# Performance work log

Hardware: AMD Instinct MI355X
Metric: run time of the kernel (lower is better)

## Reference

```python
import jax, jax.numpy as jnp
import numpy as np

B, D, G, L = 8, 128, 2048, 24
GF = G // 2 + 1  # rfft bins
EPS = 1e-5


def setup_inputs() -> dict:
    key = jax.random.key(0)
    ks = jax.random.split(key, 6)
    x = jax.random.normal(ks[0], (B, D, G), dtype=jnp.float32)
    Phi_f = jax.random.normal(ks[1], (L, GF), dtype=jnp.float32) * 0.1
    Theta = jax.random.normal(ks[2], (L, D, D), dtype=jnp.float32) * (1.0 / np.sqrt(D))
    ln_gamma = jnp.ones((D,), dtype=jnp.float32)
    ln_beta = jnp.zeros((D,), dtype=jnp.float32)
    fc1_w = jax.random.normal(ks[3], (2 * D, D), dtype=jnp.float32) * (1.0 / np.sqrt(D))
    fc1_b = jnp.zeros((2 * D,), dtype=jnp.float32)
    fc2_w = jax.random.normal(ks[4], (D, 2 * D), dtype=jnp.float32) * (1.0 / np.sqrt(2 * D))
    fc2_b = jnp.zeros((D,), dtype=jnp.float32)
    return {
        'x': x, 'Phi_f': Phi_f, 'Theta': Theta,
        'ln_gamma': ln_gamma, 'ln_beta': ln_beta,
        'fc1_w': fc1_w, 'fc1_b': fc1_b, 'fc2_w': fc2_w, 'fc2_b': fc2_b,
    }


def reference(x, Phi_f, Theta, ln_gamma, ln_beta, fc1_w, fc1_b, fc2_w, fc2_b):
    # x: (B, D, G). LayerNorm over the lifting (channel) dim D.
    mean = jnp.mean(x, axis=1, keepdims=True)
    var = jnp.var(x, axis=1, keepdims=True)
    z = (x - mean) * jax.lax.rsqrt(var + EPS)
    z = z * ln_gamma[None, :, None] + ln_beta[None, :, None]

    # Spectral convolution with each Hilbert filter.
    Xf = jnp.fft.rfft(z, axis=-1)                       # (B, D, GF) complex
    Uf = Xf[:, :, None, :] * jnp.conj(Phi_f)[None, None]  # (B, D, L, GF)
    U = jnp.fft.irfft(Uf, n=G, axis=-1)                 # (B, D, L, G)

    # Per-filter channel mixing then reduction over filters:
    # einsum('bdln,lhd->bhln') followed by sum over l, fused:
    S = jnp.einsum('bdlg,lhd->bhg', U, Theta)           # (B, D, G)

    # Pointwise MLP (Conv1d kernel_size=1 == channel matmul).
    H = jnp.einsum('hd,bdg->bhg', fc1_w, S) + fc1_b[None, :, None]
    H = jax.nn.gelu(H, approximate=False)
    out = jnp.einsum('dh,bhg->bdg', fc2_w, H) + fc2_b[None, :, None]
    return x + out
```

## Files before the change

kernel.cpp:

```cpp
#include <hip/hip_runtime.h>
#include <math.h>


#define B_   8
#define D_   128
#define G_   2048
#define L_   24
#define GF_  1025
#define BD_  1024
#define DD_  16384
#define GH_  1024
#define CF_  1026
#define MF_  1088
#define MFW_ 1152
#define NF_  2048

#define PA_CV0 256
#define PA_TT0 322
#define PA_WF0 578
#define PA_WI0 1730
#define PA_END 2754

#define G1_NB  288
#define G1_END 4512

typedef __attribute__((ext_vector_type(8))) short  short8v;
typedef __attribute__((ext_vector_type(4))) float  float4v;

union FU { float f; unsigned int u; };
union V8 { short8v v; ushort u[8]; };
union V4 { uint2 p; ushort u[4]; };

static __device__ __forceinline__ float bf2f(ushort h) {
    FU v; v.u = ((unsigned int)h) << 16; return v.f;
}
static __device__ __forceinline__ ushort f2bf(float f) {
    FU v; v.f = f;
    unsigned int r = v.u + 0x7fffu + ((v.u >> 16) & 1u);
    return (ushort)(r >> 16);
}
static __device__ __forceinline__ void async16(const void* g, void* l) {
    __builtin_amdgcn_global_load_lds(
        (const __attribute__((address_space(1))) void*)g,
        (__attribute__((address_space(3))) void*)l, 16, 0, 0);
}
static __device__ __forceinline__ int is_f32(const unsigned int* graw) {
    return graw[0] == 0x3F800000u;
}

__global__ __launch_bounds__(256) void k_pre(
        const void* __restrict__ x_raw,  const void* __restrict__ th_raw,
        const unsigned int* __restrict__ graw, const void* __restrict__ be_raw,
        const void* __restrict__ w1_raw, const void* __restrict__ b1_raw,
        const void* __restrict__ w2_raw, const void* __restrict__ b2_raw,
        ushort* __restrict__ z,  ushort* __restrict__ wf,
        ushort* __restrict__ wi, ushort* __restrict__ thT,
        ushort* __restrict__ w1c, ushort* __restrict__ b1c,
        ushort* __restrict__ w2c, ushort* __restrict__ b2c) {
    __shared__ ushort T[L_][72];
    __shared__ float red[2][256];
    __shared__ float mi[2][64];
    int bid = blockIdx.x, tid = threadIdx.x;

    if (bid < PA_CV0) {
        int fl = is_f32(graw);
        int b  = bid >> 5;
        int g0 = (bid & 31) * 64;
        int gi = tid & 63, dq = tid >> 6;
        int g  = g0 + gi;
        int d0 = dq * 32;
        float vals[32];
        float s = 0.f, ss = 0.f;
        if (fl) {
            const float* xp = (const float*)x_raw + (size_t)(b * D_ + d0) * G_ + g;
            #pragma unroll 8
            for (int d = 0; d < 32; ++d) {
                float v = xp[(size_t)d * G_];
                vals[d] = v; s += v; ss += v * v;
            }
        } else {
            const ushort* xp = (const ushort*)x_raw + (size_t)(b * D_ + d0) * G_ + g;
            #pragma unroll 8
            for (int d = 0; d < 32; ++d) {
                float v = bf2f(xp[(size_t)d * G_]);
                vals[d] = v; s += v; ss += v * v;
            }
        }
        red[0][tid] = s; red[1][tid] = ss;
        __syncthreads();
        if (tid < 64) {
            float S  = red[0][tid] + red[0][tid + 64] + red[0][tid + 128] +
                       red[0][tid + 192];
            float SS = red[1][tid] + red[1][tid + 64] + red[1][tid + 128] +
                       red[1][tid + 192];
            float mean = S * (1.f / D_);
            float var  = SS * (1.f / D_) - mean * mean;
            mi[0][tid] = mean;
            mi[1][tid] = rsqrtf(var + 1e-5f);
        }
        __syncthreads();
        float mean = mi[0][gi], inv = mi[1][gi];
        ushort* zp = z + (size_t)(g & 1) * (BD_ * GH_) +
                     (size_t)(b * D_ + d0) * GH_ + (g >> 1);
        if (fl) {
            const float* gp = (const float*)graw + d0;
            const float* bp = (const float*)be_raw + d0;
            #pragma unroll 8
            for (int d = 0; d < 32; ++d) {
                float o = (vals[d] - mean) * inv * gp[d] + bp[d];
                zp[(size_t)d * GH_] = f2bf(o);
            }
        } else {
            const ushort* gp = (const ushort*)graw + d0;
            const ushort* bp = (const ushort*)be_raw + d0;
            #pragma unroll 8
            for (int d = 0; d < 32; ++d) {
                float o = (vals[d] - mean) * inv * bf2f(gp[d]) + bf2f(bp[d]);
                zp[(size_t)d * GH_] = f2bf(o);
            }
        }
    } else if (bid < PA_TT0) {
        int fl = is_f32(graw);
        int lb = bid - PA_CV0;
        const void* src; ushort* dst; int n, rel;
        if (lb < 32)       { src = w1_raw; dst = w1c; n = 32768; rel = lb; }
        else if (lb == 32) { src = b1_raw; dst = b1c; n = 256;   rel = 0; }
        else if (lb < 65)  { src = w2_raw; dst = w2c; n = 32768; rel = lb - 33; }
        else               { src = b2_raw; dst = b2c; n = 128;   rel = 0; }
        int i0 = rel * 1024 + tid * 4;
        if (fl) {
            const float* s = (const float*)src;
            #pragma unroll
            for (int j = 0; j < 4; ++j) {
                int k = i0 + j;
                if (k < n) dst[k] = f2bf(s[k]);
            }
        } else {
            const ushort* s = (const ushort*)src;
            #pragma unroll
            for (int j = 0; j < 4; ++j) {
                int k = i0 + j;
                if (k < n) dst[k] = s[k];
            }
        }
    } else if (bid < PA_WF0) {
        int fl = is_f32(graw);
        int hd0 = (bid - PA_TT0) * 64;
        if (tid < 192) {
            int l = tid >> 3, c8 = tid & 7;
            V8 o;
            if (fl) {
                const float* tp = (const float*)th_raw + (size_t)l * DD_ +
                                  hd0 + c8 * 8;
                float4v a0 = *(const float4v*)tp;
                float4v a1 = *(const float4v*)(tp + 4);
                #pragma unroll
                for (int j = 0; j < 4; ++j) {
                    o.u[j] = f2bf(a0[j]); o.u[4 + j] = f2bf(a1[j]);
                }
            } else {
                o.v = *(const short8v*)((const ushort*)th_raw +
                                        (size_t)l * DD_ + hd0 + c8 * 8);
            }
            *(short8v*)&T[l][c8 * 8] = o.v;
        }
        __syncthreads();
        int hdl = tid & 63, part = tid >> 6;
        V8 o;
        #pragma unroll
        for (int j = 0; j < 8; ++j) {
            int l = part * 8 + j;
            o.u[j] = (l < L_) ? T[l][hdl] : (ushort)0;
        }
        *(short8v*)(thT + (size_t)(hd0 + hdl) * 32 + part * 8) = o.v;
    } else if (bid < PA_WI0) {
        int c  = bid - PA_WF0;
        int g0 = tid * 4;
        V4 v;
        if (c >= CF_) {
            #pragma unroll
            for (int j = 0; j < 4; ++j) v.u[j] = 0;
        } else {
            int f = c >> 1, im = c & 1;
            #pragma unroll
            for (int j = 0; j < 4; ++j) {
                int g = g0 + j;
                int r = (f * g) & (GH_ - 1);
                float th = (float)r * 6.135923151542565e-3f;
                v.u[j] = f2bf(im ? -__sinf(th) : __cosf(th));
            }
        }
        *(uint2*)(wf + (size_t)c * GH_ + g0) = v.p;
    } else {
        int g = bid - PA_WI0;
        for (int ch = tid; ch < MF_ / 8; ch += 256) {
            int c0 = ch * 8;
            V8 v;
            #pragma unroll
            for (int j = 0; j < 8; ++j) {
                int c = c0 + j;
                if (c >= CF_) { v.u[j] = 0; continue; }
                int f = c >> 1, im = c & 1;
                float a = (f == 0 || f == GH_ / 2) ? (1.f / 2048.f)
                                                   : (1.f / 1024.f);
                int r = (f * g) & (GH_ - 1);
                float th = (float)r * 6.135923151542565e-3f;
                v.u[j] = f2bf(im ? -a * __sinf(th) : a * __cosf(th));
            }
            *(short8v*)(wi + (size_t)g * MF_ + c0) = v.v;
        }
    }
}

__global__ __launch_bounds__(256, 3) void k_g1(
        const ushort* __restrict__ wf, const ushort* __restrict__ z,
        float* __restrict__ zft,
        const void* __restrict__ phi_raw, const unsigned int* __restrict__ graw,
        const ushort* __restrict__ thT, ushort* __restrict__ M) {
    __shared__ ushort As[2][128 * 64];
    __shared__ ushort Bs[2][64 * 64];
    __shared__ ushort Aph[16][40];
    int bid = blockIdx.x, tid = threadIdx.x;
    int w = tid >> 6, lane = tid & 63;
    int lr = lane & 15, q = lane >> 4;

    if (bid < G1_NB) {
        int m0 = (bid >> 5) * 128;
        int n0 = (bid & 31) * 64;
        int wm = (w & 1) * 64, wn = (w >> 1) * 32;
        int rl = lane >> 3, c8 = (lane & 7) ^ rl;
        int ta = w * 4, tb = w * 2;
        const ushort* gA0 = wf + (size_t)(m0 + (ta    ) * 8 + rl) * GH_ + c8 * 8;
        const ushort* gA1 = wf + (size_t)(m0 + (ta + 1) * 8 + rl) * GH_ + c8 * 8;
        const ushort* gA2 = wf + (size_t)(m0 + (ta + 2) * 8 + rl) * GH_ + c8 * 8;
        const ushort* gA3 = wf + (size_t)(m0 + (ta + 3) * 8 + rl) * GH_ + c8 * 8;
        const ushort* gB0 = z  + (size_t)(n0 + (tb    ) * 8 + rl) * GH_ + c8 * 8;
        const ushort* gB1 = z  + (size_t)(n0 + (tb + 1) * 8 + rl) * GH_ + c8 * 8;

        float4v acc[4][2];
        #pragma unroll
        for (int i = 0; i < 4; ++i)
            #pragma unroll
            for (int j = 0; j < 2; ++j) {
                float4v zz = {0.f, 0.f, 0.f, 0.f}; acc[i][j] = zz;
            }

        async16(gA0, &As[0][(ta    ) * 512]);
        async16(gA1, &As[0][(ta + 1) * 512]);
        async16(gA2, &As[0][(ta + 2) * 512]);
        async16(gA3, &As[0][(ta + 3) * 512]);
        async16(gB0, &Bs[0][(tb    ) * 512]);
        async16(gB1, &Bs[0][(tb + 1) * 512]);
        __syncthreads();

        int buf = 0;
        for (int k0 = 0; k0 < GH_; k0 += 64) {
            if (k0 + 64 < GH_) {
                int nb = buf ^ 1;
                async16(gA0 + k0 + 64, &As[nb][(ta    ) * 512]);
                async16(gA1 + k0 + 64, &As[nb][(ta + 1) * 512]);
                async16(gA2 + k0 + 64, &As[nb][(ta + 2) * 512]);
                async16(gA3 + k0 + 64, &As[nb][(ta + 3) * 512]);
                async16(gB0 + k0 + 64, &Bs[nb][(tb    ) * 512]);
                async16(gB1 + k0 + 64, &Bs[nb][(tb + 1) * 512]);
            }
            const ushort* Ab = &As[buf][0];
            const ushort* Bb = &Bs[buf][0];
            #pragma unroll
            for (int s = 0; s < 2; ++s) {
                int cs = s * 4 + q;
                int rb0 = wn + lr, rb1 = wn + 16 + lr;
                short8v b0 = *(const short8v*)(Bb + rb0 * 64 + ((cs ^ (rb0 & 7)) << 3));
                short8v b1 = *(const short8v*)(Bb + rb1 * 64 + ((cs ^ (rb1 & 7)) << 3));
                #pragma unroll
                for (int i = 0; i < 4; ++i) {
                    int ra = wm + i * 16 + lr;
                    short8v a = *(const short8v*)(Ab + ra * 64 + ((cs ^ (ra & 7)) << 3));
                    acc[i][0] = __builtin_amdgcn_mfma_f32_16x16x32_bf16(a, b0, acc[i][0], 0, 0, 0);
                    acc[i][1] = __builtin_amdgcn_mfma_f32_16x16x32_bf16(a, b1, acc[i][1], 0, 0, 0);
                }
            }
            __syncthreads();
            buf ^= 1;
        }

        #pragma unroll
        for (int i = 0; i < 4; ++i)
            #pragma unroll
            for (int j = 0; j < 2; ++j) {
                int col = n0 + wn + j * 16 + lr;
                int row = m0 + wm + i * 16 + q * 4;
                #pragma unroll
                for (int r = 0; r < 4; ++r)
                    zft[(size_t)(row + r) * NF_ + col] = acc[i][j][r];
            }
    } else {
        int bb  = bid - G1_NB;
        int f0  = (bb >> 6) * 16;
        int hd0 = (bb & 63) * 256;
        int isf = is_f32(graw);
        #pragma unroll
        for (int rep = 0; rep < 2; ++rep) {
            int idx = rep * 256 + tid;
            int fl = idx >> 5, l = idx & 31;
            int f = f0 + fl;
            ushort v = 0;
            if (l < L_ && f < GF_)
                v = isf ? f2bf(((const float*)phi_raw)[(size_t)l * GF_ + f])
                        : ((const ushort*)phi_raw)[(size_t)l * GF_ + f];
            Aph[fl][l] = v;
        }
        __syncthreads();
        short8v a = *(const short8v*)&Aph[lr][q * 8];
        #pragma unroll
        for (int t = 0; t < 4; ++t) {
            int n = hd0 + (w * 4 + t) * 16 + lr;
            short8v b = *(const short8v*)(thT + (size_t)n * 32 + q * 8);
            float4v c = {0.f, 0.f, 0.f, 0.f};
            c = __builtin_amdgcn_mfma_f32_16x16x32_bf16(a, b, c, 0, 0, 0);
            #pragma unroll
            for (int r = 0; r < 4; ++r) {
                int f = f0 + q * 4 + r;
                if (f < GF_) M[(size_t)f * DD_ + n] = f2bf(c[r]);
            }
        }
    }
}

__global__ __launch_bounds__(256, 2) void k_mix3(const float* __restrict__ zft,
                                                 const ushort* __restrict__ M,
                                                 ushort* __restrict__ sft) {
    int fp  = blockIdx.x;
    int fb  = GH_ - fp;
    int tid = threadIdx.x;
    int w = tid >> 6, lane = tid & 63;
    int lr = lane & 15, q = lane >> 4;
    int cc = lr >> 3, bb = lr & 7;

    float ang = (float)fp * 3.0679615757712823e-3f;
    float wr  = cosf(ang), sn = sinf(ang);
    float wi_ = -sn;
    float wsig = cc ? wi_ : -wi_;
    float cbv  = cc ? wr  : -wr;
    float asgn = cc ? -1.f : 1.f;

    const float* rc = zft + (size_t)(2 * fp + cc) * NF_;
    const float* ro = zft + (size_t)(2 * fp + (cc ^ 1)) * NF_;
    int colb = bb * 128 + q * 8;

    short8v aZ[4], aZb[4];
    #pragma unroll
    for (int s = 0; s < 4; ++s) {
        int col = colb + s * 32;
        float4v av0 = *(const float4v*)(rc + col);
        float4v av1 = *(const float4v*)(rc + col + 4);
        float4v bv0 = *(const float4v*)(rc + BD_ + col);
        float4v bv1 = *(const float4v*)(rc + BD_ + col + 4);
        float4v bo0 = *(const float4v*)(ro + BD_ + col);
        float4v bo1 = *(const float4v*)(ro + BD_ + col + 4);
        V8 tz, tb;
        #pragma unroll
        for (int j = 0; j < 4; ++j) {
            float av = av0[j], bv = bv0[j], bo = bo0[j];
            float zz = fmaf(wsig, bo, fmaf(wr, bv, av));
            float zb = fmaf(cbv, bv, fmaf(wi_, bo, asgn * av));
            tz.u[j] = f2bf(zz); tb.u[j] = f2bf(zb);
            av = av1[j]; bv = bv1[j]; bo = bo1[j];
            zz = fmaf(wsig, bo, fmaf(wr, bv, av));
            zb = fmaf(cbv, bv, fmaf(wi_, bo, asgn * av));
            tz.u[4 + j] = f2bf(zz); tb.u[4 + j] = f2bf(zb);
        }
        aZ[s] = tz.v; aZb[s] = tb.v;
    }

    const ushort* Mf = M + (size_t)fp * DD_;
    const ushort* Mb = M + (size_t)fb * DD_;
    #pragma unroll
    for (int n = 0; n < 2; ++n) {
        int nt = 2 * w + n;
        float4v c1 = {0.f, 0.f, 0.f, 0.f};
        float4v c2 = {0.f, 0.f, 0.f, 0.f};
        #pragma unroll
        for (int s = 0; s < 4; ++s) {
            short8v b1 = *(const short8v*)(Mf + (size_t)(nt * 16 + lr) * D_ +
                                           s * 32 + q * 8);
            short8v b2 = *(const short8v*)(Mb + (size_t)(nt * 16 + lr) * D_ +
                                           s * 32 + q * 8);
            c1 = __builtin_amdgcn_mfma_f32_16x16x32_bf16(aZ[s],  b1, c1, 0, 0, 0);
            c2 = __builtin_amdgcn_mfma_f32_16x16x32_bf16(aZb[s], b2, c2, 0, 0, 0);
        }
        #pragma unroll
        for (int r = 0; r < 4; ++r) {
            int p   = q * 4 + r;
            int c2i = p >> 3, b2 = p & 7;
            float sgm = c2i ? -1.f : 1.f;
            float se  = c1[r] + sgm * c2[r];
            float sop = c1[r] - sgm * c2[r];
            float pp  = __shfl_xor(sop, 32);
            float tsg = c2i ? sn : -sn;
            float so  = fmaf(tsg, pp, sop * wr);
            size_t rowo = (size_t)(2 * fp + c2i) * NF_;
            int colh = b2 * 128 + nt * 16 + lr;
            sft[rowo + colh]       = f2bf(se);
            sft[rowo + BD_ + colh] = f2bf(so);
        }
    }
}

__global__ __launch_bounds__(256, 4) void k_gemm64t(const ushort* __restrict__ A,
                                                    const ushort* __restrict__ Bm,
                                                    ushort* __restrict__ C,
                                                    int K, int lda, int ldb,
                                                    int ldc, int kv) {
    __shared__ ushort As[2][64 * 64];
    __shared__ ushort Bs[2][64 * 64];
    int tid = threadIdx.x;
    int m0 = blockIdx.x * 64, n0 = blockIdx.y * 64;
    int w = tid >> 6, lane = tid & 63;
    int lr = lane & 15, q = lane >> 4;
    int wm = (w & 1) * 32, wn = (w >> 1) * 32;

    int rl = lane >> 3, c8 = (lane & 7) ^ rl;
    int t0 = w * 2, t1 = w * 2 + 1;
    const ushort* gA0 = A + (size_t)(m0 + t0 * 8 + rl) * lda + c8 * 8;
    const ushort* gA1 = A + (size_t)(m0 + t1 * 8 + rl) * lda + c8 * 8;

    int br = tid >> 2;
    int bc = tid & 3;

    float4v acc00 = {0.f,0.f,0.f,0.f}, acc01 = {0.f,0.f,0.f,0.f};
    float4v acc10 = {0.f,0.f,0.f,0.f}, acc11 = {0.f,0.f,0.f,0.f};

    async16(gA0, &As[0][t0 * 512]);
    async16(gA1, &As[0][t1 * 512]);
    {
        V8 u0, u1;
        if (br < kv) {
            const ushort* gb = Bm + (size_t)br * ldb + n0 + bc * 16;
            u0.v = *(const short8v*)gb;
            u1.v = *(const short8v*)(gb + 8);
        } else {
            #pragma unroll
            for (int j = 0; j < 8; ++j) { u0.u[j] = 0; u1.u[j] = 0; }
        }
        #pragma unroll
        for (int j = 0; j < 8; ++j) {
            int n = bc * 16 + j;
            Bs[0][n * 64 + ((((br >> 3) ^ (n & 7)) << 3) | (br & 7))] = u0.u[j];
        }
        #pragma unroll
        for (int j = 0; j < 8; ++j) {
            int n = bc * 16 + 8 + j;
            Bs[0][n * 64 + ((((br >> 3) ^ (n & 7)) << 3) | (br & 7))] = u1.u[j];
        }
    }
    __syncthreads();

    int buf = 0;
    for (int k0 = 0; k0 < K; k0 += 64) {
        V8 u0, u1;
        bool more = (k0 + 64 < K);
        if (more) {
            int nb = buf ^ 1;
            async16(gA0 + k0 + 64, &As[nb][t0 * 512]);
            async16(gA1 + k0 + 64, &As[nb][t1 * 512]);
            int kr = k0 + 64 + br;
            if (kr < kv) {
                const ushort* gb = Bm + (size_t)kr * ldb + n0 + bc * 16;
                u0.v = *(const short8v*)gb;
                u1.v = *(const short8v*)(gb + 8);
            } else {
                #pragma unroll
                for (int j = 0; j < 8; ++j) { u0.u[j] = 0; u1.u[j] = 0; }
            }
        }
        const ushort* Ab = &As[buf][0];
        const ushort* Bb = &Bs[buf][0];
        #pragma unroll
        for (int s = 0; s < 2; ++s) {
            int cs = s * 4 + q;
            int ra0 = wm + lr, ra1 = wm + 16 + lr;
            int rb0 = wn + lr, rb1 = wn + 16 + lr;
            short8v a0 = *(const short8v*)(Ab + ra0 * 64 + ((cs ^ (ra0 & 7)) << 3));
            short8v a1 = *(const short8v*)(Ab + ra1 * 64 + ((cs ^ (ra1 & 7)) << 3));
            short8v b0 = *(const short8v*)(Bb + rb0 * 64 + ((cs ^ (rb0 & 7)) << 3));
            short8v b1 = *(const short8v*)(Bb + rb1 * 64 + ((cs ^ (rb1 & 7)) << 3));
            acc00 = __builtin_amdgcn_mfma_f32_16x16x32_bf16(a0, b0, acc00, 0, 0, 0);
            acc01 = __builtin_amdgcn_mfma_f32_16x16x32_bf16(a0, b1, acc01, 0, 0, 0);
            acc10 = __builtin_amdgcn_mfma_f32_16x16x32_bf16(a1, b0, acc10, 0, 0, 0);
            acc11 = __builtin_amdgcn_mfma_f32_16x16x32_bf16(a1, b1, acc11, 0, 0, 0);
        }
        __syncthreads();
        if (more) {
            int nb = buf ^ 1;
            #pragma unroll
            for (int j = 0; j < 8; ++j) {
                int n = bc * 16 + j;
                Bs[nb][n * 64 + ((((br >> 3) ^ (n & 7)) << 3) | (br & 7))] = u0.u[j];
            }
            #pragma unroll
            for (int j = 0; j < 8; ++j) {
                int n = bc * 16 + 8 + j;
                Bs[nb][n * 64 + ((((br >> 3) ^ (n & 7)) << 3) | (br & 7))] = u1.u[j];
            }
        }
        __syncthreads();
        buf ^= 1;
    }

    float4v accs[2][2] = { { acc00, acc01 }, { acc10, acc11 } };
    #pragma unroll
    for (int i = 0; i < 2; ++i)
        #pragma unroll
        for (int j = 0; j < 2; ++j) {
            int col = n0 + wn + j * 16 + lr;
            int row = m0 + wm + i * 16 + q * 4;
            #pragma unroll
            for (int r = 0; r < 4; ++r)
                C[(size_t)(row + r) * ldc + col] = f2bf(accs[i][j][r]);
        }
}

#define MLPG 32
__global__ __launch_bounds__(256, 2) void k_mlp3(const ushort* __restrict__ ST,
                                                 const void* __restrict__ x0,
                                                 const ushort* __restrict__ w1,
                                                 const ushort* __restrict__ b1,
                                                 const ushort* __restrict__ w2,
                                                 const ushort* __restrict__ b2,
                                                 const unsigned int* __restrict__ graw,
                                                 void* __restrict__ outv) {
    __shared__ ushort Sb[MLPG][136];
    __shared__ ushort Hb[MLPG][264];
    __shared__ float  Ob[128][36];
    int g0 = blockIdx.x * MLPG, b = blockIdx.y;
    int tid = threadIdx.x;
    {
        int col = tid >> 3, seg = tid & 7;
        int g = g0 + col;
        const ushort* sp = ST + (size_t)(g >> 1) * NF_ + (g & 1) * BD_ +
                           b * D_ + seg * 16;
        short8v s0 = *(const short8v*)(sp);
        short8v s1 = *(const short8v*)(sp + 8);
        *(short8v*)&Sb[col][seg * 16]     = s0;
        *(short8v*)&Sb[col][seg * 16 + 8] = s1;
    }
    __syncthreads();
    int w = tid >> 6, lane = tid & 63;
    int lr = lane & 15, q = lane >> 4;
    int nt = w & 1, mh = w >> 1;

    {
        float4v acc[8];
        #pragma unroll
        for (int i = 0; i < 8; ++i) { float4v zz = {0.f,0.f,0.f,0.f}; acc[i] = zz; }
        #pragma unroll
        for (int ks = 0; ks < 4; ++ks) {
            short8v bf = *(const short8v*)&Sb[nt * 16 + lr][ks * 32 + q * 8];
            #pragma unroll
            for (int i = 0; i < 8; ++i) {
                int mt = mh * 8 + i;
                short8v af = *(const short8v*)(w1 + (size_t)(mt * 16 + lr) * D_ +
                                               ks * 32 + q * 8);
                acc[i] = __builtin_amdgcn_mfma_f32_16x16x32_bf16(af, bf, acc[i], 0, 0, 0);
            }
        }
        #pragma unroll
        for (int i = 0; i < 8; ++i) {
            int h0 = (mh * 8 + i) * 16 + q * 4;
            V4 hv;
            #pragma unroll
            for (int r = 0; r < 4; ++r) {
                float v = acc[i][r] + bf2f(b1[h0 + r]);
                v = 0.5f * v * (1.f + erff(v * 0.70710678118f));
                hv.u[r] = f2bf(v);
            }
            *(uint2*)&Hb[nt * 16 + lr][h0] = hv.p;
        }
    }
    __syncthreads();
    {
        float4v acc2[4];
        #pragma unroll
        for (int j = 0; j < 4; ++j) { float4v zz = {0.f,0.f,0.f,0.f}; acc2[j] = zz; }
        #pragma unroll
        for (int ks = 0; ks < 8; ++ks) {
            short8v bf = *(const short8v*)&Hb[nt * 16 + lr][ks * 32 + q * 8];
            #pragma unroll
            for (int j = 0; j < 4; ++j) {
                int mt2 = mh * 4 + j;
                short8v af = *(const short8v*)(w2 + (size_t)(mt2 * 16 + lr) * (2 * D_) +
                                               ks * 32 + q * 8);
                acc2[j] = __builtin_amdgcn_mfma_f32_16x16x32_bf16(af, bf, acc2[j], 0, 0, 0);
            }
        }
        int col = nt * 16 + lr;
        #pragma unroll
        for (int j = 0; j < 4; ++j) {
            int d0 = (mh * 4 + j) * 16 + q * 4;
            #pragma unroll
            for (int r = 0; r < 4; ++r)
                Ob[d0 + r][col] = acc2[j][r] + bf2f(b2[d0 + r]);
        }
    }
    __syncthreads();
    {
        int fl = is_f32(graw);
        if (fl) {
            #pragma unroll
            for (int p = 0; p < 4; ++p) {
                int idx = p * 256 + tid;
                int d = idx >> 3, c4 = (idx & 7) * 4;
                float4v o = *(const float4v*)&Ob[d][c4];
                size_t gidx = ((size_t)(b * D_ + d)) * G_ + g0 + c4;
                float4v xv = *(const float4v*)((const float*)x0 + gidx);
                float4v ov;
                #pragma unroll
                for (int k = 0; k < 4; ++k) ov[k] = o[k] + xv[k];
                *(float4v*)((float*)outv + gidx) = ov;
            }
        } else {
            #pragma unroll
            for (int p = 0; p < 4; ++p) {
                int idx = p * 256 + tid;
                int d = idx >> 3, c4 = (idx & 7) * 4;
                float4v o = *(const float4v*)&Ob[d][c4];
                size_t gidx = ((size_t)(b * D_ + d)) * G_ + g0 + c4;
                V4 xv; xv.p = *(const uint2*)((const ushort*)x0 + gidx);
                V4 ov;
                #pragma unroll
                for (int k = 0; k < 4; ++k) ov.u[k] = f2bf(o[k] + bf2f(xv.u[k]));
                *(uint2*)((ushort*)outv + gidx) = ov.p;
            }
        }
    }
}

extern "C" void kernel_launch(void* const* d_in, const int* in_sizes, int n_in,
                              void* d_out, int out_size, void* d_ws, size_t ws_size,
                              hipStream_t stream) {
    char* base = (char*)d_ws;
    ushort* z    = (ushort*)(base);
    ushort* wf   = (ushort*)(base + 4194304);
    ushort* sft  = (ushort*)(base);
    float*  zft  = (float*)(base + 13107200);
    ushort* st   = (ushort*)(base + 13107200);
    ushort* w1c  = (ushort*)(base + 27050048);
    ushort* b1c  = (ushort*)(base + 27115584);
    ushort* w2c  = (ushort*)(base + 27116096);
    ushort* b2c  = (ushort*)(base + 27181632);
    ushort* Mm   = (ushort*)(base + 27182592);
    ushort* wi   = (ushort*)(base + 60769792);
    ushort* thT  = (ushort*)(base + 69420544);

    const unsigned int* graw = (const unsigned int*)d_in[3];

    k_pre    <<<dim3(PA_END), 256, 0, stream>>>(
        d_in[0], d_in[2], graw, d_in[4], d_in[5], d_in[6], d_in[7], d_in[8],
        z, wf, wi, thT, w1c, b1c, w2c, b2c);
    k_g1     <<<dim3(G1_END), 256, 0, stream>>>(wf, z, zft, d_in[1], graw,
                                                thT, Mm);
    k_mix3   <<<dim3(513), 256, 0, stream>>>(zft, Mm, sft);
    k_gemm64t<<<dim3(GH_ / 64, NF_ / 64), 256, 0, stream>>>(
        wi, sft, st, MF_, MF_, NF_, NF_, CF_);
    k_mlp3   <<<dim3(G_ / MLPG, B_), 256, 0, stream>>>(st, d_in[0], w1c, b1c,
                                                       w2c, b2c, graw, d_out);
}
```

Measured before the change: 166.9 us.

## Store forward DFT output as bf16 and shrink GEMM tile to 64x64

The forward-DFT GEMM in k_g1 now writes its output zft as bf16 instead of fp32, which halves that intermediate's write traffic and k_mix3's read traffic. k_mix3 now loads 8 bf16 values per vector load. The GEMM tile is reduced from 128x64 to 64x64, which doubles the block count, halves LDS use, and raises launch bounds to 4 waves per SIMD. The k_pre block ranges shift to match the smaller wf buffer. The cost is an extra bf16 rounding of the spectral coefficients and less data reuse per GEMM tile.

Result: faster. 160.8 us (-3.7%).

```diff
diff --git a/kernel.cpp b/kernel.cpp
--- a/kernel.cpp
+++ b/kernel.cpp
@@ -12,17 +12,16 @@
 #define GH_  1024
 #define CF_  1026
 #define MF_  1088
-#define MFW_ 1152
 #define NF_  2048
 
 #define PA_CV0 256
 #define PA_TT0 322
 #define PA_WF0 578
-#define PA_WI0 1730
-#define PA_END 2754
-
-#define G1_NB  288
-#define G1_END 4512
+#define PA_WI0 1666
+#define PA_END 2690
+
+#define G1_NB  544
+#define G1_END 4768
 
 typedef __attribute__((ext_vector_type(8))) short  short8v;
 typedef __attribute__((ext_vector_type(4))) float  float4v;
@@ -212,12 +211,12 @@
     }
 }
 
-__global__ __launch_bounds__(256, 3) void k_g1(
+__global__ __launch_bounds__(256, 4) void k_g1(
         const ushort* __restrict__ wf, const ushort* __restrict__ z,
-        float* __restrict__ zft,
+        ushort* __restrict__ zft,
         const void* __restrict__ phi_raw, const unsigned int* __restrict__ graw,
         const ushort* __restrict__ thT, ushort* __restrict__ M) {
-    __shared__ ushort As[2][128 * 64];
+    __shared__ ushort As[2][64 * 64];
     __shared__ ushort Bs[2][64 * 64];
     __shared__ ushort Aph[16][40];
     int bid = blockIdx.x, tid = threadIdx.x;
@@ -225,74 +224,64 @@
     int lr = lane & 15, q = lane >> 4;
 
     if (bid < G1_NB) {
-        int m0 = (bid >> 5) * 128;
+        int m0 = (bid >> 5) * 64;
         int n0 = (bid & 31) * 64;
-        int wm = (w & 1) * 64, wn = (w >> 1) * 32;
+        int wm = (w & 1) * 32, wn = (w >> 1) * 32;
         int rl = lane >> 3, c8 = (lane & 7) ^ rl;
-        int ta = w * 4, tb = w * 2;
-        const ushort* gA0 = wf + (size_t)(m0 + (ta    ) * 8 + rl) * GH_ + c8 * 8;
-        const ushort* gA1 = wf + (size_t)(m0 + (ta + 1) * 8 + rl) * GH_ + c8 * 8;
-        const ushort* gA2 = wf + (size_t)(m0 + (ta + 2) * 8 + rl) * GH_ + c8 * 8;
-        const ushort* gA3 = wf + (size_t)(m0 + (ta + 3) * 8 + rl) * GH_ + c8 * 8;
-        const ushort* gB0 = z  + (size_t)(n0 + (tb    ) * 8 + rl) * GH_ + c8 * 8;
-        const ushort* gB1 = z  + (size_t)(n0 + (tb + 1) * 8 + rl) * GH_ + c8 * 8;
-
-        float4v acc[4][2];
-        #pragma unroll
-        for (int i = 0; i < 4; ++i)
-            #pragma unroll
-            for (int j = 0; j < 2; ++j) {
-                float4v zz = {0.f, 0.f, 0.f, 0.f}; acc[i][j] = zz;
-            }
-
-        async16(gA0, &As[0][(ta    ) * 512]);
-        async16(gA1, &As[0][(ta + 1) * 512]);
-        async16(gA2, &As[0][(ta + 2) * 512]);
-        async16(gA3, &As[0][(ta + 3) * 512]);
-        async16(gB0, &Bs[0][(tb    ) * 512]);
-        async16(gB1, &Bs[0][(tb + 1) * 512]);
+        int t0 = w * 2, t1 = w * 2 + 1;
+        const ushort* gA0 = wf + (size_t)(m0 + t0 * 8 + rl) * GH_ + c8 * 8;
+        const ushort* gA1 = wf + (size_t)(m0 + t1 * 8 + rl) * GH_ + c8 * 8;
+        const ushort* gB0 = z  + (size_t)(n0 + t0 * 8 + rl) * GH_ + c8 * 8;
+        const ushort* gB1 = z  + (size_t)(n0 + t1 * 8 + rl) * GH_ + c8 * 8;
+
+        float4v acc00 = {0.f,0.f,0.f,0.f}, acc01 = {0.f,0.f,0.f,0.f};
+        float4v acc10 = {0.f,0.f,0.f,0.f}, acc11 = {0.f,0.f,0.f,0.f};
+
+        async16(gA0, &As[0][t0 * 512]);
+        async16(gA1, &As[0][t1 * 512]);
+        async16(gB0, &Bs[0][t0 * 512]);
+        async16(gB1, &Bs[0][t1 * 512]);
         __syncthreads();
 
         int buf = 0;
         for (int k0 = 0; k0 < GH_; k0 += 64) {
             if (k0 + 64 < GH_) {
                 int nb = buf ^ 1;
-                async16(gA0 + k0 + 64, &As[nb][(ta    ) * 512]);
-                async16(gA1 + k0 + 64, &As[nb][(ta + 1) * 512]);
-                async16(gA2 + k0 + 64, &As[nb][(ta + 2) * 512]);
-                async16(gA3 + k0 + 64, &As[nb][(ta + 3) * 512]);
-                async16(gB0 + k0 + 64, &Bs[nb][(tb    ) * 512]);
-                async16(gB1 + k0 + 64, &Bs[nb][(tb + 1) * 512]);
+                async16(gA0 + k0 + 64, &As[nb][t0 * 512]);
+                async16(gA1 + k0 + 64, &As[nb][t1 * 512]);
+                async16(gB0 + k0 + 64, &Bs[nb][t0 * 512]);
+                async16(gB1 + k0 + 64, &Bs[nb][t1 * 512]);
             }
             const ushort* Ab = &As[buf][0];
             const ushort* Bb = &Bs[buf][0];
             #pragma unroll
             for (int s = 0; s < 2; ++s) {
                 int cs = s * 4 + q;
+                int ra0 = wm + lr, ra1 = wm + 16 + lr;
                 int rb0 = wn + lr, rb1 = wn + 16 + lr;
+                short8v a0 = *(const short8v*)(Ab + ra0 * 64 + ((cs ^ (ra0 & 7)) << 3));
+                short8v a1 = *(const short8v*)(Ab + ra1 * 64 + ((cs ^ (ra1 & 7)) << 3));
                 short8v b0 = *(const short8v*)(Bb + rb0 * 64 + ((cs ^ (rb0 & 7)) << 3));
                 short8v b1 = *(const short8v*)(Bb + rb1 * 64 + ((cs ^ (rb1 & 7)) << 3));
-                #pragma unroll
-                for (int i = 0; i < 4; ++i) {
-                    int ra = wm + i * 16 + lr;
-                    short8v a = *(const short8v*)(Ab + ra * 64 + ((cs ^ (ra & 7)) << 3));
-                    acc[i][0] = __builtin_amdgcn_mfma_f32_16x16x32_bf16(a, b0, acc[i][0], 0, 0, 0);
-                    acc[i][1] = __builtin_amdgcn_mfma_f32_16x16x32_bf16(a, b1, acc[i][1], 0, 0, 0);
-                }
+                acc00 = __builtin_amdgcn_mfma_f32_16x16x32_bf16(a0, b0, acc00, 0, 0, 0);
+                acc01 = __builtin_amdgcn_mfma_f32_16x16x32_bf16(a0, b1, acc01, 0, 0, 0);
+                acc10 = __builtin_amdgcn_mfma_f32_16x16x32_bf16(a1, b0, acc10, 0, 0, 0);
+                acc11 = __builtin_amdgcn_mfma_f32_16x16x32_bf16(a1, b1, acc11, 0, 0, 0);
             }
             __syncthreads();
             buf ^= 1;
         }
 
-        #pragma unroll
-        for (int i = 0; i < 4; ++i)
+        float4v accs[2][2] = { { acc00, acc01 }, { acc10, acc11 } };
+        #pragma unroll
+        for (int i = 0; i < 2; ++i)
             #pragma unroll
             for (int j = 0; j < 2; ++j) {
                 int col = n0 + wn + j * 16 + lr;
                 int row = m0 + wm + i * 16 + q * 4;
                 #pragma unroll
                 for (int r = 0; r < 4; ++r)
-                    zft[(size_t)(row + r) * NF_ + col] = acc[i][j][r];
+                    zft[(size_t)(row + r) * NF_ + col] = f2bf(accs[i][j][r]);
             }
     } else {
         int bb  = bid - G1_NB;
@@ -327,7 +316,7 @@
     }
 }
 
-__global__ __launch_bounds__(256, 2) void k_mix3(const float* __restrict__ zft,
+__global__ __launch_bounds__(256, 2) void k_mix3(const ushort* __restrict__ zft,
                                                  const ushort* __restrict__ M,
                                                  ushort* __restrict__ sft) {
     int fp  = blockIdx.x;
@@ -344,31 +333,25 @@
     float cbv  = cc ? wr  : -wr;
     float asgn = cc ? -1.f : 1.f;
 
-    const float* rc = zft + (size_t)(2 * fp + cc) * NF_;
-    const float* ro = zft + (size_t)(2 * fp + (cc ^ 1)) * NF_;
+    const ushort* rc = zft + (size_t)(2 * fp + cc) * NF_;
+    const ushort* ro = zft + (size_t)(2 * fp + (cc ^ 1)) * NF_;
     int colb = bb * 128 + q * 8;
 
     short8v aZ[4], aZb[4];
     #pragma unroll
     for (int s = 0; s < 4; ++s) {
         int col = colb + s * 32;
-        float4v av0 = *(const float4v*)(rc + col);
-        float4v av1 = *(const float4v*)(rc + col + 4);
-        float4v bv0 = *(const float4v*)(rc + BD_ + col);
-        float4v bv1 = *(const float4v*)(rc + BD_ + col + 4);
-        float4v bo0 = *(const float4v*)(ro + BD_ + col);
-        float4v bo1 = *(const float4v*)(ro + BD_ + col + 4);
+        V8 aU, bU, oU;
+        aU.v = *(const short8v*)(rc + col);
+        bU.v = *(const short8v*)(rc + BD_ + col);
+        oU.v = *(const short8v*)(ro + BD_ + col);
         V8 tz, tb;
         #pragma unroll
-        for (int j = 0; j < 4; ++j) {
-            float av = av0[j], bv = bv0[j], bo = bo0[j];
+        for (int j = 0; j < 8; ++j) {
+            float av = bf2f(aU.u[j]), bv = bf2f(bU.u[j]), bo = bf2f(oU.u[j]);
             float zz = fmaf(wsig, bo, fmaf(wr, bv, av));
             float zb = fmaf(cbv, bv, fmaf(wi_, bo, asgn * av));
             tz.u[j] = f2bf(zz); tb.u[j] = f2bf(zb);
-            av = av1[j]; bv = bv1[j]; bo = bo1[j];
-            zz = fmaf(wsig, bo, fmaf(wr, bv, av));
-            zb = fmaf(cbv, bv, fmaf(wi_, bo, asgn * av));
-            tz.u[4 + j] = f2bf(zz); tb.u[4 + j] = f2bf(zb);
         }
         aZ[s] = tz.v; aZb[s] = tb.v;
     }
@@ -643,7 +626,7 @@
     ushort* z    = (ushort*)(base);
     ushort* wf   = (ushort*)(base + 4194304);
     ushort* sft  = (ushort*)(base);
-    float*  zft  = (float*)(base + 13107200);
+    ushort* zft  = (ushort*)(base + 13107200);
     ushort* st   = (ushort*)(base + 13107200);
     ushort* w1c  = (ushort*)(base + 27050048);
     ushort* b1c  = (ushort*)(base + 27115584);
```
